# Optimization experiments

Measured on AMD Instinct MI355X. Metric: run time of the kernel, lower is better.

## Reference

```python
import jax, jax.numpy as jnp
import numpy as np

N_VARS = 6
N_SAMPLES = 16384
N_SETS = 4  # per variable; n_rules = N_SETS ** N_VARS = 4096


def setup_inputs() -> dict:
    key = jax.random.key(0)
    memberships = jax.random.uniform(key, (N_VARS, N_SAMPLES, N_SETS), dtype=jnp.float32)
    return {"memberships": memberships}


def reference(memberships) -> jnp.ndarray:
    # Antecedents over the full Cartesian product of fuzzy sets with the
    # product t-norm as AND. itertools.product iterates the LAST variable's
    # set index fastest, which is exactly row-major reshape order, so we can
    # build the [N, R] rule activations as a chained outer product instead of
    # looping over all R rules.
    n_vars = memberships.shape[0]
    acc = memberships[0]  # [N, n0]
    for v in range(1, n_vars):  # small fixed loop over variables (6)
        N = acc.shape[0]
        # [N, r, 1] * [N, 1, nv] -> [N, r*nv]
        acc = (acc[:, :, None] * memberships[v][:, None, :]).reshape(N, -1)
    return acc  # [N, n_rules]
```

## Files before the change

kernel.cpp:

```cpp
#include <hip/hip_runtime.h>


constexpr int N_VARS    = 6;
constexpr int N_SAMPLES = 16384;
constexpr int N_SETS    = 4;
constexpr int N_COMBOS  = 1024;

typedef float v4f __attribute__((ext_vector_type(4)));

__global__ __launch_bounds__(256) void antecedents_kernel(
    const float* __restrict__ m, v4f* __restrict__ out4) {
  const int n = blockIdx.x;
  const int t = threadIdx.x;

  __shared__ __align__(16) float sm[N_VARS][N_SETS];
  if (t < N_VARS * N_SETS) {
    const int v = t >> 2, s = t & 3;
    sm[v][s] = m[(size_t)v * (N_SAMPLES * N_SETS) + (size_t)n * N_SETS + s];
  }
  __syncthreads();

  const int s1 = (t >> 6) & 3;
  const int s2 = (t >> 4) & 3;
  const int s3 = (t >> 2) & 3;
  const int s4 = t & 3;

  const float q = sm[1][s1] * sm[2][s2] * sm[3][s3] * sm[4][s4];
  const v4f m5 = *reinterpret_cast<const v4f*>(&sm[5][0]);

  v4f* dst = out4 + (size_t)n * N_COMBOS + t;
#pragma unroll
  for (int i = 0; i < 4; ++i) {
    const float p = sm[0][i] * q;
    dst[i * 256] = p * m5;
  }
}

extern "C" void kernel_launch(void* const* d_in, const int* in_sizes, int n_in,
                              void* d_out, int out_size, void* d_ws, size_t ws_size,
                              hipStream_t stream) {
  const float* m = (const float*)d_in[0];
  v4f* out = (v4f*)d_out;
  antecedents_kernel<<<N_SAMPLES, 256, 0, stream>>>(m, out);
}
```

Measured before the change: 256.6 us.

## Process eight samples per block and drop shared-memory staging

Each block now handles eight samples instead of one, with every thread loading the six membership vectors directly as broadcast float4 loads and picking elements by register select. The shared-memory staging and the barrier go away. The aim is to cut block launch and sync overhead on a kernel that is bound by output writes. In exchange there are fewer blocks in the grid and more redundant global loads per thread, which should mostly hit in cache.

```diff
diff --git a/kernel.cpp b/kernel.cpp
--- a/kernel.cpp
+++ b/kernel.cpp
@@ -1,38 +1,49 @@
 #include <hip/hip_runtime.h>
 
 
-constexpr int N_VARS    = 6;
 constexpr int N_SAMPLES = 16384;
 constexpr int N_SETS    = 4;
-constexpr int N_COMBOS  = 1024;
+constexpr int SPB       = 8;
+constexpr int VSTRIDE   = N_SAMPLES * N_SETS;
 
 typedef float v4f __attribute__((ext_vector_type(4)));
 
+__device__ __forceinline__ float sel4(v4f v, int i) {
+  float r = v.x;
+  r = (i == 1) ? v.y : r;
+  r = (i == 2) ? v.z : r;
+  r = (i == 3) ? v.w : r;
+  return r;
+}
+
 __global__ __launch_bounds__(256) void antecedents_kernel(
     const float* __restrict__ m, v4f* __restrict__ out4) {
-  const int n = blockIdx.x;
-  const int t = threadIdx.x;
-
-  __shared__ __align__(16) float sm[N_VARS][N_SETS];
-  if (t < N_VARS * N_SETS) {
-    const int v = t >> 2, s = t & 3;
-    sm[v][s] = m[(size_t)v * (N_SAMPLES * N_SETS) + (size_t)n * N_SETS + s];
-  }
-  __syncthreads();
+  const int t  = threadIdx.x;
+  const int n0 = blockIdx.x * SPB;
 
   const int s1 = (t >> 6) & 3;
   const int s2 = (t >> 4) & 3;
   const int s3 = (t >> 2) & 3;
   const int s4 = t & 3;
 
-  const float q = sm[1][s1] * sm[2][s2] * sm[3][s3] * sm[4][s4];
-  const v4f m5 = *reinterpret_cast<const v4f*>(&sm[5][0]);
+#pragma unroll
+  for (int j = 0; j < SPB; ++j) {
+    const int n = n0 + j;
+    const v4f m0 = *reinterpret_cast<const v4f*>(m + 0 * VSTRIDE + n * N_SETS);
+    const v4f m1 = *reinterpret_cast<const v4f*>(m + 1 * VSTRIDE + n * N_SETS);
+    const v4f m2 = *reinterpret_cast<const v4f*>(m + 2 * VSTRIDE + n * N_SETS);
+    const v4f m3 = *reinterpret_cast<const v4f*>(m + 3 * VSTRIDE + n * N_SETS);
+    const v4f m4 = *reinterpret_cast<const v4f*>(m + 4 * VSTRIDE + n * N_SETS);
+    const v4f m5 = *reinterpret_cast<const v4f*>(m + 5 * VSTRIDE + n * N_SETS);
 
-  v4f* dst = out4 + (size_t)n * N_COMBOS + t;
-#pragma unroll
-  for (int i = 0; i < 4; ++i) {
-    const float p = sm[0][i] * q;
-    dst[i * 256] = p * m5;
+    const float q = sel4(m1, s1) * sel4(m2, s2) * sel4(m3, s3) * sel4(m4, s4);
+    const v4f qm5 = q * m5;
+
+    v4f* dst = out4 + (size_t)n * 1024 + t;
+    dst[0]   = m0.x * qm5;
+    dst[256] = m0.y * qm5;
+    dst[512] = m0.z * qm5;
+    dst[768] = m0.w * qm5;
   }
 }
 
@@ -41,5 +52,5 @@
                               hipStream_t stream) {
   const float* m = (const float*)d_in[0];
   v4f* out = (v4f*)d_out;
-  antecedents_kernel<<<N_SAMPLES, 256, 0, stream>>>(m, out);
+  antecedents_kernel<<<N_SAMPLES / SPB, 256, 0, stream>>>(m, out);
 }
```

New measurement: 258.3 us. Within noise of the previous version (+0.6%).
